# Kernel tuning notes

Hardware: AMD Instinct MI355X
Metric: run time of the kernel (lower is better)

Reference implementation:

```python
import jax, jax.numpy as jnp
import numpy as np

BLOCK_SIZE = 64


def setup_inputs() -> dict:
    key = jax.random.key(0)
    kq, kk, kv, km = jax.random.split(key, 4)
    H, N, D = 16, 8192, 64
    nb = N // BLOCK_SIZE
    return {
        "q": jax.random.normal(kq, (H, N, D), dtype=jnp.float32),
        "k": jax.random.normal(kk, (H, N, D), dtype=jnp.float32),
        "v": jax.random.normal(kv, (H, N, D), dtype=jnp.float32),
        "block_mask": jax.random.randint(km, (nb, nb), 0, 2, dtype=jnp.int32),
    }


def reference(q, k, v, block_mask):
    """Block-sparse flash attention with online softmax.

    q, k, v: [H, N, D]; block_mask: [N//B, N//B] (1 = valid, 0 = masked).
    Scans over key blocks, processing all query rows at once; masked blocks
    contribute exactly zero (exp(-inf) = 0), matching the original's skip.
    """
    H, N, D = q.shape
    B = BLOCK_SIZE
    nb = N // B
    scale = D ** -0.5

    kb = k.reshape(H, nb, B, D).transpose(1, 0, 2, 3)  # [nb, H, B, D]
    vb = v.reshape(H, nb, B, D).transpose(1, 0, 2, 3)  # [nb, H, B, D]
    mask_cols = block_mask.T  # [nb_key, nb_query]: row j = validity of key block j per query block

    m0 = jnp.full((H, N, 1), -jnp.inf, dtype=q.dtype)
    l0 = jnp.zeros((H, N, 1), dtype=q.dtype)
    o0 = jnp.zeros((H, N, D), dtype=q.dtype)

    def step(carry, xs):
        m, l, o = carry
        k_j, v_j, mcol = xs  # k_j/v_j: [H, B, D]; mcol: [nb] over query blocks
        logits = jnp.einsum('hnd,hbd->hnb', q, k_j) * scale  # [H, N, B]
        valid = (jnp.repeat(mcol, B) > 0)[None, :, None]      # [1, N, 1]
        logits = jnp.where(valid, logits, -jnp.inf)
        m_new = jnp.maximum(m, logits.max(-1, keepdims=True))
        # guard: if everything so far is masked, m_new = -inf; use 0 to keep exps finite (=0)
        m_safe = jnp.where(jnp.isneginf(m_new), jnp.zeros_like(m_new), m_new)
        a_old = jnp.exp(m - m_safe)       # rescale of previous accumulators
        p = jnp.exp(logits - m_safe)      # masked entries -> 0
        l = a_old * l + p.sum(-1, keepdims=True)
        o = a_old * o + jnp.einsum('hnb,hbd->hnd', p, v_j)
        return (m_new, l, o), None

    (m, l, o), _ = jax.lax.scan(step, (m0, l0, o0), (kb, vb, mask_cols))
    return o / l
```

## Files before the change

### kernel.cpp

```cpp
#include <hip/hip_runtime.h>
#include <hip/hip_bf16.h>

#define Hh 16
#define Nn 8192
#define Dd 64
#define NB 128

typedef float  f32x4   __attribute__((ext_vector_type(4)));
typedef float  f32x16  __attribute__((ext_vector_type(16)));
typedef float  float4_ __attribute__((ext_vector_type(4)));
typedef short  bf16x8  __attribute__((ext_vector_type(8)));
typedef unsigned short ushort8  __attribute__((ext_vector_type(8)));
typedef unsigned short ushort4_ __attribute__((ext_vector_type(4)));

typedef const __attribute__((address_space(1))) unsigned int gu32;
typedef __attribute__((address_space(3))) unsigned int lu32;

#define QSCALE 0.1803368801111244f

__device__ __forceinline__ unsigned short f2bf(float f) {
    union { float f; unsigned u; } x; x.f = f;
    unsigned r = x.u + 0x7fffu + ((x.u >> 16) & 1u);
    return (unsigned short)(r >> 16);
}

__device__ __forceinline__ unsigned packbf2(float lo, float hi) {
    __hip_bfloat162 h2 = __float22bfloat162_rn(make_float2(lo, hi));
    unsigned u; __builtin_memcpy(&u, &h2, 4);
    return u;
}

__global__ void cvt_k(const float* __restrict__ k, unsigned short* __restrict__ ko) {
    int i = blockIdx.x * 256 + threadIdx.x;
    float4_ b = ((const float4_*)k)[i];
    ushort4_ ob;
#pragma unroll
    for (int j = 0; j < 4; ++j) ob[j] = f2bf(b[j]);
    ((ushort4_*)ko)[i] = ob;
}

__global__ void cvt_vt(const float* __restrict__ v, unsigned short* __restrict__ vt) {
    int jb = blockIdx.x, h = blockIdx.y, t = threadIdx.x;
    __shared__ float T[64][65];
    const float4_* src = (const float4_*)(v + ((long)h * Nn + jb * 64) * Dd);
#pragma unroll
    for (int it = 0; it < 4; ++it) {
        int r = (t >> 4) + it * 16;
        int c0 = (t & 15) * 4;
        float4_ x = src[r * 16 + (t & 15)];
#pragma unroll
        for (int i2 = 0; i2 < 4; ++i2) T[c0 + i2][r] = x[i2];
    }
    __syncthreads();
    int d = t >> 2, seg = (t & 3) * 16;
    ushort8 o0, o1;
#pragma unroll
    for (int i2 = 0; i2 < 8; ++i2) o0[i2] = f2bf(T[d][seg + i2]);
#pragma unroll
    for (int i2 = 0; i2 < 8; ++i2) o1[i2] = f2bf(T[d][seg + 8 + i2]);
    unsigned short* dst = vt + (((size_t)h * NB + jb) * Dd + d) * 64 + seg;
    *(ushort8*)dst = o0;
    *(ushort8*)(dst + 8) = o1;
}

__global__ __launch_bounds__(256, 2) void attn32(
        const unsigned short* __restrict__ k16,
        const unsigned short* __restrict__ vt16,
        const float* __restrict__ qf,
        const int* __restrict__ mask,
        float* __restrict__ out) {
    int bid = blockIdx.x;
    int h = (bid & 7) | ((bid >> 9) << 3);
    int qb2 = (bid >> 3) & 63;
    int tid = threadIdx.x;
    int wid = tid >> 6, l = tid & 63;
    int q5 = l & 31, hi = l >> 5;
    int pair = wid >> 1;
    int kvrole = wid & 1;

    __shared__ unsigned short Kl[2][2][4096];
    __shared__ unsigned short Vl[2][2][4096];

    const int* mrowA = mask + (qb2 * 2) * NB;
    const int* mrowB = mask + (qb2 * 2 + 1) * NB;
    unsigned long long a_lo = __ballot(mrowA[l] != 0);
    unsigned long long a_hi = __ballot(mrowA[64 + l] != 0);
    unsigned long long c_lo = __ballot(mrowB[l] != 0);
    unsigned long long c_hi = __ballot(mrowB[64 + l] != 0);
    int cntA = __popcll(a_lo) + __popcll(a_hi);
    int cntB = __popcll(c_lo) + __popcll(c_hi);
    int maxcnt = cntA > cntB ? cntA : cntB;

    if (maxcnt == 0) {
        float4_ z = {0.f, 0.f, 0.f, 0.f};
        float4_* ob = (float4_*)(out + ((size_t)h * Nn + qb2 * 128) * Dd);
        for (int x = tid; x < 128 * 64 / 4; x += 256) ob[x] = z;
        return;
    }

    int cnt_own = pair ? cntB : cntA;
    unsigned long long r0 = pair ? c_lo : a_lo;
    unsigned long long r1 = pair ? c_hi : a_hi;

    size_t qrow = (size_t)h * Nn + qb2 * 128 + pair * 64 + kvrole * 32 + q5;
    bf16x8 qfrag[4];
#pragma unroll
    for (int ds_ = 0; ds_ < 4; ++ds_) {
        const float4_* qs = (const float4_*)(qf + qrow * Dd + ds_ * 16 + hi * 8);
        float4_ x = qs[0], y = qs[1];
        union { unsigned u[4]; bf16x8 v; } u;
        u.u[0] = packbf2(x[0] * QSCALE, x[1] * QSCALE);
        u.u[1] = packbf2(x[2] * QSCALE, x[3] * QSCALE);
        u.u[2] = packbf2(y[0] * QSCALE, y[1] * QSCALE);
        u.u[3] = packbf2(y[2] * QSCALE, y[3] * QSCALE);
        qfrag[ds_] = u.v;
    }

    union { unsigned short s[8]; bf16x8 v; } ones;
#pragma unroll
    for (int i2 = 0; i2 < 8; ++i2) ones.s[i2] = 0x3F80;

    const unsigned short* sp[8];
#pragma unroll
    for (int f = 0; f < 8; ++f) {
        if (kvrole == 0)
            sp[f] = k16 + (size_t)h * (Nn * Dd)
                  + (size_t)(q5 + 32 * (f >> 2)) * Dd + (f & 3) * 16 + hi * 8;
        else
            sp[f] = vt16 + (size_t)h * (Nn * Dd)
                  + (size_t)(q5 + 32 * (f >> 2)) * 64 + (f & 3) * 16 + hi * 8;
    }
    const int jmul = 64 * Dd;

    auto next_j = [&]() {
        int jj;
        if (r0)      { jj = __ffsll(r0) - 1; r0 &= r0 - 1; }
        else if (r1) { jj = 63 + __ffsll(r1); r1 &= r1 - 1; }
        else         { jj = 0; }
        return jj;
    };

    auto issue = [&](int nbuf, int jj) {
        unsigned short* lb = (kvrole == 0) ? &Kl[pair][nbuf][0] : &Vl[pair][nbuf][0];
#pragma unroll
        for (int f = 0; f < 8; ++f) {
            const unsigned short* g = sp[f] + (size_t)jj * jmul;
            __builtin_amdgcn_global_load_lds((gu32*)g, (lu32*)(lb + f * 512), 16, 0, 0);
        }
    };

    issue(0, next_j());

    f32x16 o0 = {}, o1 = {}, ls = {};

    for (int i = 0; i < maxcnt; ++i) {
        int buf = i & 1;
        __syncthreads();
        if (i + 1 < maxcnt) issue(buf ^ 1, next_j());

        unsigned msk = (i < cnt_own) ? 0xFFFFFFFFu : 0u;

        const char* kb = (const char*)&Kl[pair][buf][0] + l * 16;
        const char* vb = (const char*)&Vl[pair][buf][0] + l * 16;

        f32x16 s0 = {}, s1 = {};
#pragma unroll
        for (int ds_ = 0; ds_ < 4; ++ds_) {
            bf16x8 kf0 = *(const bf16x8*)(kb + ds_ * 1024);
            s0 = __builtin_amdgcn_mfma_f32_32x32x16_bf16(kf0, qfrag[ds_], s0, 0, 0, 0);
        }
#pragma unroll
        for (int ds_ = 0; ds_ < 4; ++ds_) {
            bf16x8 kf1 = *(const bf16x8*)(kb + 4096 + ds_ * 1024);
            s1 = __builtin_amdgcn_mfma_f32_32x32x16_bf16(kf1, qfrag[ds_], s1, 0, 0, 0);
        }

#pragma unroll
        for (int e = 0; e < 16; ++e) s0[e] = __builtin_amdgcn_exp2f(s0[e]);
#pragma unroll
        for (int e = 0; e < 16; ++e) s1[e] = __builtin_amdgcn_exp2f(s1[e]);

        unsigned w0[8], w1[8];
#pragma unroll
        for (int jj = 0; jj < 8; ++jj) {
            w0[jj] = packbf2(s0[2 * jj], s0[2 * jj + 1]) & msk;
            w1[jj] = packbf2(s1[2 * jj], s1[2 * jj + 1]) & msk;
        }
        auto swap32 = [&](unsigned& a, unsigned& b) {
            unsigned send = hi ? a : b;
            unsigned recv = (unsigned)__shfl_xor((int)send, 32);
            a = hi ? recv : a;
            b = hi ? b : recv;
        };
        swap32(w0[0], w0[2]); swap32(w0[1], w0[3]);
        swap32(w0[4], w0[6]); swap32(w0[5], w0[7]);
        swap32(w1[0], w1[2]); swap32(w1[1], w1[3]);
        swap32(w1[4], w1[6]); swap32(w1[5], w1[7]);

        union U { unsigned u[4]; bf16x8 v; };
        U pbs[4];
        pbs[0].u[0] = w0[0]; pbs[0].u[1] = w0[1]; pbs[0].u[2] = w0[2]; pbs[0].u[3] = w0[3];
        pbs[1].u[0] = w0[4]; pbs[1].u[1] = w0[5]; pbs[1].u[2] = w0[6]; pbs[1].u[3] = w0[7];
        pbs[2].u[0] = w1[0]; pbs[2].u[1] = w1[1]; pbs[2].u[2] = w1[2]; pbs[2].u[3] = w1[3];
        pbs[3].u[0] = w1[4]; pbs[3].u[1] = w1[5]; pbs[3].u[2] = w1[6]; pbs[3].u[3] = w1[7];

#pragma unroll
        for (int c = 0; c < 4; ++c) {
            bf16x8 vf0 = *(const bf16x8*)(vb + c * 1024);
            o0 = __builtin_amdgcn_mfma_f32_32x32x16_bf16(vf0, pbs[c].v, o0, 0, 0, 0);
        }
#pragma unroll
        for (int c = 0; c < 4; ++c) {
            bf16x8 vf1 = *(const bf16x8*)(vb + 4096 + c * 1024);
            o1 = __builtin_amdgcn_mfma_f32_32x32x16_bf16(vf1, pbs[c].v, o1, 0, 0, 0);
        }
#pragma unroll
        for (int c = 0; c < 4; ++c)
            ls = __builtin_amdgcn_mfma_f32_32x32x16_bf16(ones.v, pbs[c].v, ls, 0, 0, 0);
    }

    float inv = cnt_own ? (1.0f / ls[0]) : 0.f;
    float* obase = out + qrow * Dd;
#pragma unroll
    for (int s4 = 0; s4 < 4; ++s4) {
        float4_ t0, t1;
#pragma unroll
        for (int e = 0; e < 4; ++e) { t0[e] = o0[4 * s4 + e] * inv; t1[e] = o1[4 * s4 + e] * inv; }
        *(float4_*)(obase + 8 * s4 + 4 * hi)      = t0;
        *(float4_*)(obase + 32 + 8 * s4 + 4 * hi) = t1;
    }
}

__global__ void attn_main(const float* __restrict__ qf, const float* __restrict__ kf,
                          const float* __restrict__ vf, const int* __restrict__ mask,
                          float* __restrict__ out) {
    int id = blockIdx.x;
    int h = id & 15, qb = id >> 4;
    int tid = threadIdx.x;
    int lane = tid & 63, wid = tid >> 6;
    int l15 = lane & 15, l4 = lane >> 4;

    __shared__ unsigned short Kl[2][64 * 64];
    __shared__ unsigned short Vl[2][64 * 64];
    __shared__ unsigned short Pl[4][16 * 64];

    const int* mrow = mask + qb * NB;
    unsigned long long b0 = __ballot(mrow[lane] != 0);
    unsigned long long b1 = __ballot(mrow[64 + lane] != 0);
    int count = __popcll(b0) + __popcll(b1);

    float* op = out + ((long)h * Nn + qb * 64 + wid * 16) * Dd;

    if (count == 0) {
#pragma unroll
        for (int r = 0; r < 4; ++r)
#pragma unroll
            for (int dn = 0; dn < 4; ++dn)
                op[(l4 * 4 + r) * Dd + dn * 16 + l15] = 0.f;
        return;
    }

    long qrow = (long)h * Nn + qb * 64 + wid * 16 + l15;
    bf16x8 qfrag[2];
#pragma unroll
    for (int dc = 0; dc < 2; ++dc) {
        const float4_* qs = (const float4_*)qf + qrow * 16 + dc * 8 + l4 * 2;
        float4_ x = qs[0], y = qs[1];
        union { unsigned short s[8]; bf16x8 v; } u;
#pragma unroll
        for (int i2 = 0; i2 < 4; ++i2) {
            u.s[i2] = f2bf(x[i2] * 0.125f);
            u.s[4 + i2] = f2bf(y[i2] * 0.125f);
        }
        qfrag[dc] = u.v;
    }

    int sgq = tid & 7;
    int srow = tid >> 3;
    float4_ kf4[2][2]; float4_ vf4[4];
    int vk = tid & 63, vd0 = (tid >> 6) * 16;

    auto load_kv = [&](int j) {
        const float4_* ks = (const float4_*)kf + ((long)h * Nn + j * 64) * 16;
#pragma unroll
        for (int it = 0; it < 2; ++it) {
            kf4[it][0] = ks[(srow + it * 32) * 16 + sgq * 2];
            kf4[it][1] = ks[(srow + it * 32) * 16 + sgq * 2 + 1];
        }
        const float4_* vs = (const float4_*)vf + ((long)h * Nn + j * 64) * 16;
#pragma unroll
        for (int c = 0; c < 4; ++c) vf4[c] = vs[vk * 16 + (vd0 >> 2) + c];
    };

    auto write_kv = [&](int buf) {
#pragma unroll
        for (int it = 0; it < 2; ++it) {
            int r = srow + it * 32;
            union { unsigned short s[8]; ushort8 v; } u;
#pragma unroll
            for (int i2 = 0; i2 < 4; ++i2) {
                u.s[i2] = f2bf(kf4[it][0][i2]);
                u.s[4 + i2] = f2bf(kf4[it][1][i2]);
            }
            *(ushort8*)((char*)&Kl[buf][0] + r * 128 + (((sgq ^ r) & 7) << 4)) = u.v;
        }
#pragma unroll
        for (int i2 = 0; i2 < 16; ++i2) {
            int d = vd0 + i2;
            *((unsigned short*)((char*)&Vl[buf][0] + d * 128 +
                ((((vk >> 3) ^ d) & 7) << 4) + ((vk & 7) << 1))) = f2bf(vf4[i2 >> 2][i2 & 3]);
        }
    };

    f32x4 o_acc[4] = {};
    float m_r[4], l_r[4];
#pragma unroll
    for (int r = 0; r < 4; ++r) { m_r[r] = -INFINITY; l_r[r] = 0.f; }

    unsigned long long r0 = b0, r1 = b1;
    auto next_j = [&]() {
        int jj;
        if (r0) { jj = __ffsll(r0) - 1; r0 &= r0 - 1; }
        else    { jj = 63 + __ffsll(r1); r1 &= r1 - 1; }
        return jj;
    };

    load_kv(next_j());

    for (int i = 0; i < count; ++i) {
        int buf = i & 1;
        write_kv(buf);
        __syncthreads();
        if (i + 1 < count) load_kv(next_j());

        f32x4 s[4] = {};
#pragma unroll
        for (int dc = 0; dc < 2; ++dc) {
#pragma unroll
            for (int kn = 0; kn < 4; ++kn) {
                int krow = kn * 16 + l15;
                bf16x8 kfr = *(const bf16x8*)((const char*)&Kl[buf][0] +
                               krow * 128 + ((((l4 + dc * 4) ^ krow) & 7) << 4));
                s[kn] = __builtin_amdgcn_mfma_f32_16x16x32_bf16(qfrag[dc], kfr, s[kn], 0, 0, 0);
            }
        }

#pragma unroll
        for (int r = 0; r < 4; ++r) {
            float mx = fmaxf(fmaxf(s[0][r], s[1][r]), fmaxf(s[2][r], s[3][r]));
#pragma unroll
            for (int off = 1; off < 16; off <<= 1) mx = fmaxf(mx, __shfl_xor(mx, off));
            float mn = fmaxf(m_r[r], mx);
            float a = __expf(m_r[r] - mn);
            m_r[r] = mn;
            float psum = 0.f;
#pragma unroll
            for (int kn = 0; kn < 4; ++kn) { float p = __expf(s[kn][r] - mn); s[kn][r] = p; psum += p; }
#pragma unroll
            for (int off = 1; off < 16; off <<= 1) psum += __shfl_xor(psum, off);
            l_r[r] = l_r[r] * a + psum;
            o_acc[0][r] *= a; o_acc[1][r] *= a; o_acc[2][r] *= a; o_acc[3][r] *= a;
        }

#pragma unroll
        for (int kn = 0; kn < 4; ++kn) {
#pragma unroll
            for (int r = 0; r < 4; ++r) {
                int prow = l4 * 4 + r;
                int pc = kn * 16 + l15;
                *((unsigned short*)((char*)&Pl[wid][0] + prow * 128 +
                    ((((pc >> 3) ^ prow) & 7) << 4) + ((pc & 7) << 1))) = f2bf(s[kn][r]);
            }
        }

        bf16x8 pa[2];
#pragma unroll
        for (int kc = 0; kc < 2; ++kc)
            pa[kc] = *(const bf16x8*)((const char*)&Pl[wid][0] +
                      l15 * 128 + ((((l4 + kc * 4) ^ l15) & 7) << 4));
#pragma unroll
        for (int dn = 0; dn < 4; ++dn) {
            int vrow = dn * 16 + l15;
#pragma unroll
            for (int kc = 0; kc < 2; ++kc) {
                bf16x8 vbf = *(const bf16x8*)((const char*)&Vl[buf][0] +
                             vrow * 128 + ((((l4 + kc * 4) ^ vrow) & 7) << 4));
                o_acc[dn] = __builtin_amdgcn_mfma_f32_16x16x32_bf16(pa[kc], vbf, o_acc[dn], 0, 0, 0);
            }
        }
    }

#pragma unroll
    for (int r = 0; r < 4; ++r) {
        float inv = 1.0f / l_r[r];
#pragma unroll
        for (int dn = 0; dn < 4; ++dn)
            op[(l4 * 4 + r) * Dd + dn * 16 + l15] = o_acc[dn][r] * inv;
    }
}

extern "C" void kernel_launch(void* const* d_in, const int* in_sizes, int n_in,
                              void* d_out, int out_size, void* d_ws, size_t ws_size,
                              hipStream_t stream) {
    const float* q = (const float*)d_in[0];
    const float* k = (const float*)d_in[1];
    const float* v = (const float*)d_in[2];
    const int* mask = (const int*)d_in[3];
    float* out = (float*)d_out;

    size_t elems = (size_t)Hh * Nn * Dd;
    size_t need = 2 * elems * sizeof(unsigned short);
    if (ws_size >= need) {
        unsigned short* k16 = (unsigned short*)d_ws;
        unsigned short* vt16 = k16 + elems;
        cvt_k<<<dim3((unsigned)(elems / 1024)), 256, 0, stream>>>(k, k16);
        cvt_vt<<<dim3(NB, Hh), 256, 0, stream>>>(v, vt16);
        attn32<<<dim3(Hh * NB / 2), 256, 0, stream>>>(k16, vt16, q, mask, out);
    } else {
        attn_main<<<dim3(Hh * NB), 256, 0, stream>>>(q, k, v, mask, out);
    }
}
```

Before: 288.9 us.

## Split attention blocks to one query block per workgroup, drop LDS double buffering

Each 128-thread workgroup now handles a single 64-row query block instead of two paired blocks in a 256-thread workgroup. This removes the padding work that occurs when two query blocks have different mask counts. The K/V tiles now use a single LDS buffer, with the next load issued after compute and a second barrier. That gives up the overlap between the next tile's load and the current MFMA work in exchange for less LDS, smaller workgroups and more of them resident.

```diff
diff --git a/kernel.cpp b/kernel.cpp
--- a/kernel.cpp
+++ b/kernel.cpp
@@ -63,46 +63,36 @@
     *(ushort8*)(dst + 8) = o1;
 }
 
-__global__ __launch_bounds__(256, 2) void attn32(
+__global__ __launch_bounds__(128, 4) void attn32(
         const unsigned short* __restrict__ k16,
         const unsigned short* __restrict__ vt16,
         const float* __restrict__ qf,
         const int* __restrict__ mask,
         float* __restrict__ out) {
     int bid = blockIdx.x;
-    int h = (bid & 7) | ((bid >> 9) << 3);
-    int qb2 = (bid >> 3) & 63;
+    int h = (bid & 7) | ((bid >> 10) << 3);
+    int qb = (bid >> 3) & 127;
     int tid = threadIdx.x;
     int wid = tid >> 6, l = tid & 63;
     int q5 = l & 31, hi = l >> 5;
-    int pair = wid >> 1;
-    int kvrole = wid & 1;
-
-    __shared__ unsigned short Kl[2][2][4096];
-    __shared__ unsigned short Vl[2][2][4096];
-
-    const int* mrowA = mask + (qb2 * 2) * NB;
-    const int* mrowB = mask + (qb2 * 2 + 1) * NB;
-    unsigned long long a_lo = __ballot(mrowA[l] != 0);
-    unsigned long long a_hi = __ballot(mrowA[64 + l] != 0);
-    unsigned long long c_lo = __ballot(mrowB[l] != 0);
-    unsigned long long c_hi = __ballot(mrowB[64 + l] != 0);
-    int cntA = __popcll(a_lo) + __popcll(a_hi);
-    int cntB = __popcll(c_lo) + __popcll(c_hi);
-    int maxcnt = cntA > cntB ? cntA : cntB;
-
-    if (maxcnt == 0) {
+
+    __shared__ unsigned short Kl[4096];
+    __shared__ unsigned short Vl[4096];
+
+    const int* mrow = mask + qb * NB;
+    unsigned long long b0 = __ballot(mrow[l] != 0);
+    unsigned long long b1 = __ballot(mrow[64 + l] != 0);
+    int count = __popcll(b0) + __popcll(b1);
+
+    size_t qrow = (size_t)h * Nn + qb * 64 + wid * 32 + q5;
+
+    if (count == 0) {
         float4_ z = {0.f, 0.f, 0.f, 0.f};
-        float4_* ob = (float4_*)(out + ((size_t)h * Nn + qb2 * 128) * Dd);
-        for (int x = tid; x < 128 * 64 / 4; x += 256) ob[x] = z;
+        float4_* ob = (float4_*)(out + ((size_t)h * Nn + qb * 64) * Dd);
+        for (int x = tid; x < 64 * 64 / 4; x += 128) ob[x] = z;
         return;
     }
 
-    int cnt_own = pair ? cntB : cntA;
-    unsigned long long r0 = pair ? c_lo : a_lo;
-    unsigned long long r1 = pair ? c_hi : a_hi;
-
-    size_t qrow = (size_t)h * Nn + qb2 * 128 + pair * 64 + kvrole * 32 + q5;
     bf16x8 qfrag[4];
 #pragma unroll
     for (int ds_ = 0; ds_ < 4; ++ds_) {
@@ -123,7 +113,7 @@
     const unsigned short* sp[8];
 #pragma unroll
     for (int f = 0; f < 8; ++f) {
-        if (kvrole == 0)
+        if (wid == 0)
             sp[f] = k16 + (size_t)h * (Nn * Dd)
                   + (size_t)(q5 + 32 * (f >> 2)) * Dd + (f & 3) * 16 + hi * 8;
         else
@@ -132,16 +122,16 @@
     }
     const int jmul = 64 * Dd;
 
+    unsigned long long r0 = b0, r1 = b1;
     auto next_j = [&]() {
         int jj;
-        if (r0)      { jj = __ffsll(r0) - 1; r0 &= r0 - 1; }
-        else if (r1) { jj = 63 + __ffsll(r1); r1 &= r1 - 1; }
-        else         { jj = 0; }
+        if (r0) { jj = __ffsll(r0) - 1; r0 &= r0 - 1; }
+        else    { jj = 63 + __ffsll(r1); r1 &= r1 - 1; }
         return jj;
     };
 
-    auto issue = [&](int nbuf, int jj) {
-        unsigned short* lb = (kvrole == 0) ? &Kl[pair][nbuf][0] : &Vl[pair][nbuf][0];
+    auto issue = [&](int jj) {
+        unsigned short* lb = (wid == 0) ? &Kl[0] : &Vl[0];
 #pragma unroll
         for (int f = 0; f < 8; ++f) {
             const unsigned short* g = sp[f] + (size_t)jj * jmul;
@@ -149,19 +139,15 @@
         }
     };
 
-    issue(0, next_j());
+    issue(next_j());
 
     f32x16 o0 = {}, o1 = {}, ls = {};
 
-    for (int i = 0; i < maxcnt; ++i) {
-        int buf = i & 1;
+    for (int i = 0; i < count; ++i) {
         __syncthreads();
-        if (i + 1 < maxcnt) issue(buf ^ 1, next_j());
-
-        unsigned msk = (i < cnt_own) ? 0xFFFFFFFFu : 0u;
-
-        const char* kb = (const char*)&Kl[pair][buf][0] + l * 16;
-        const char* vb = (const char*)&Vl[pair][buf][0] + l * 16;
+
+        const char* kb = (const char*)&Kl[0] + l * 16;
+        const char* vb = (const char*)&Vl[0] + l * 16;
 
         f32x16 s0 = {}, s1 = {};
 #pragma unroll
@@ -183,8 +169,8 @@
         unsigned w0[8], w1[8];
 #pragma unroll
         for (int jj = 0; jj < 8; ++jj) {
-            w0[jj] = packbf2(s0[2 * jj], s0[2 * jj + 1]) & msk;
-            w1[jj] = packbf2(s1[2 * jj], s1[2 * jj + 1]) & msk;
+            w0[jj] = packbf2(s0[2 * jj], s0[2 * jj + 1]);
+            w1[jj] = packbf2(s1[2 * jj], s1[2 * jj + 1]);
         }
         auto swap32 = [&](unsigned& a, unsigned& b) {
             unsigned send = hi ? a : b;
@@ -217,9 +203,12 @@
 #pragma unroll
         for (int c = 0; c < 4; ++c)
             ls = __builtin_amdgcn_mfma_f32_32x32x16_bf16(ones.v, pbs[c].v, ls, 0, 0, 0);
-    }
-
-    float inv = cnt_own ? (1.0f / ls[0]) : 0.f;
+
+        __syncthreads();
+        if (i + 1 < count) issue(next_j());
+    }
+
+    float inv = 1.0f / ls[0];
     float* obase = out + qrow * Dd;
 #pragma unroll
     for (int s4 = 0; s4 < 4; ++s4) {
@@ -415,7 +404,7 @@
         unsigned short* vt16 = k16 + elems;
         cvt_k<<<dim3((unsigned)(elems / 1024)), 256, 0, stream>>>(k, k16);
         cvt_vt<<<dim3(NB, Hh), 256, 0, stream>>>(v, vt16);
-        attn32<<<dim3(Hh * NB / 2), 256, 0, stream>>>(k16, vt16, q, mask, out);
+        attn32<<<dim3(Hh * NB), 128, 0, stream>>>(k16, vt16, q, mask, out);
     } else {
         attn_main<<<dim3(Hh * NB), 256, 0, stream>>>(q, k, v, mask, out);
     }
```

New measurement: 319.4 us. +10.6%, slower.

## Split key blocks into 32-key halves to halve LDS and raise occupancy

Applied to the files above, without the earlier changes.

The attn32 kernel now processes each 64-key block as two 32-key sub-steps. This halves the K/V shared-memory buffers, live score registers and P fragments, and launch bounds rise from 2 to 4 blocks per CU. The aim is more concurrent waves to hide memory and MFMA latency. The cost is twice as many loop iterations, so twice as many __syncthreads barriers and async issue points per key block, with smaller loads per step.

```diff
diff --git a/kernel.cpp b/kernel.cpp
--- a/kernel.cpp
+++ b/kernel.cpp
@@ -63,7 +63,7 @@
     *(ushort8*)(dst + 8) = o1;
 }
 
-__global__ __launch_bounds__(256, 2) void attn32(
+__global__ __launch_bounds__(256, 4) void attn32(
         const unsigned short* __restrict__ k16,
         const unsigned short* __restrict__ vt16,
         const float* __restrict__ qf,
@@ -78,8 +78,8 @@
     int pair = wid >> 1;
     int kvrole = wid & 1;
 
-    __shared__ unsigned short Kl[2][2][4096];
-    __shared__ unsigned short Vl[2][2][4096];
+    __shared__ unsigned short Kl[2][2][2048];
+    __shared__ unsigned short Vl[2][2][2048];
 
     const int* mrowA = mask + (qb2 * 2) * NB;
     const int* mrowB = mask + (qb2 * 2 + 1) * NB;
@@ -98,7 +98,8 @@
         return;
     }
 
-    int cnt_own = pair ? cntB : cntA;
+    int cnt_own2 = 2 * (pair ? cntB : cntA);
+    int maxcnt2 = 2 * maxcnt;
     unsigned long long r0 = pair ? c_lo : a_lo;
     unsigned long long r1 = pair ? c_hi : a_hi;
 
@@ -120,72 +121,68 @@
 #pragma unroll
     for (int i2 = 0; i2 < 8; ++i2) ones.s[i2] = 0x3F80;
 
-    const unsigned short* sp[8];
-#pragma unroll
-    for (int f = 0; f < 8; ++f) {
+    const unsigned short* sp[4];
+#pragma unroll
+    for (int f = 0; f < 4; ++f) {
         if (kvrole == 0)
             sp[f] = k16 + (size_t)h * (Nn * Dd)
-                  + (size_t)(q5 + 32 * (f >> 2)) * Dd + (f & 3) * 16 + hi * 8;
+                  + (size_t)q5 * Dd + f * 16 + hi * 8;
         else
             sp[f] = vt16 + (size_t)h * (Nn * Dd)
-                  + (size_t)(q5 + 32 * (f >> 2)) * 64 + (f & 3) * 16 + hi * 8;
-    }
-    const int jmul = 64 * Dd;
-
-    auto next_j = [&]() {
-        int jj;
-        if (r0)      { jj = __ffsll(r0) - 1; r0 &= r0 - 1; }
-        else if (r1) { jj = 63 + __ffsll(r1); r1 &= r1 - 1; }
-        else         { jj = 0; }
-        return jj;
+                  + (size_t)(q5 + 32 * (f >> 1)) * 64 + (f & 1) * 16 + hi * 8;
+    }
+
+    int hold_j = 0, sub = 0;
+    auto next_off = [&]() -> size_t {
+        if (sub == 0) {
+            if (r0)      { hold_j = __ffsll(r0) - 1; r0 &= r0 - 1; }
+            else if (r1) { hold_j = 63 + __ffsll(r1); r1 &= r1 - 1; }
+            else         { hold_j = 0; }
+            sub = 1;
+            return (size_t)hold_j * 4096;
+        } else {
+            sub = 0;
+            return (size_t)hold_j * 4096 + (kvrole == 0 ? 2048u : 32u);
+        }
     };
 
-    auto issue = [&](int nbuf, int jj) {
+    auto issue = [&](int nbuf, size_t off) {
         unsigned short* lb = (kvrole == 0) ? &Kl[pair][nbuf][0] : &Vl[pair][nbuf][0];
 #pragma unroll
-        for (int f = 0; f < 8; ++f) {
-            const unsigned short* g = sp[f] + (size_t)jj * jmul;
+        for (int f = 0; f < 4; ++f) {
+            const unsigned short* g = sp[f] + off;
             __builtin_amdgcn_global_load_lds((gu32*)g, (lu32*)(lb + f * 512), 16, 0, 0);
         }
     };
 
-    issue(0, next_j());
+    issue(0, next_off());
 
     f32x16 o0 = {}, o1 = {}, ls = {};
 
-    for (int i = 0; i < maxcnt; ++i) {
+    for (int i = 0; i < maxcnt2; ++i) {
         int buf = i & 1;
         __syncthreads();
-        if (i + 1 < maxcnt) issue(buf ^ 1, next_j());
-
-        unsigned msk = (i < cnt_own) ? 0xFFFFFFFFu : 0u;
+        if (i + 1 < maxcnt2) issue(buf ^ 1, next_off());
+
+        unsigned msk = (i < cnt_own2) ? 0xFFFFFFFFu : 0u;
 
         const char* kb = (const char*)&Kl[pair][buf][0] + l * 16;
         const char* vb = (const char*)&Vl[pair][buf][0] + l * 16;
 
-        f32x16 s0 = {}, s1 = {};
+        f32x16 s0 = {};
 #pragma unroll
         for (int ds_ = 0; ds_ < 4; ++ds_) {
             bf16x8 kf0 = *(const bf16x8*)(kb + ds_ * 1024);
             s0 = __builtin_amdgcn_mfma_f32_32x32x16_bf16(kf0, qfrag[ds_], s0, 0, 0, 0);
         }
-#pragma unroll
-        for (int ds_ = 0; ds_ < 4; ++ds_) {
-            bf16x8 kf1 = *(const bf16x8*)(kb + 4096 + ds_ * 1024);
-            s1 = __builtin_amdgcn_mfma_f32_32x32x16_bf16(kf1, qfrag[ds_], s1, 0, 0, 0);
-        }
 
 #pragma unroll
         for (int e = 0; e < 16; ++e) s0[e] = __builtin_amdgcn_exp2f(s0[e]);
-#pragma unroll
-        for (int e = 0; e < 16; ++e) s1[e] = __builtin_amdgcn_exp2f(s1[e]);
-
-        unsigned w0[8], w1[8];
-#pragma unroll
-        for (int jj = 0; jj < 8; ++jj) {
+
+        unsigned w0[8];
+#pragma unroll
+        for (int jj = 0; jj < 8; ++jj)
             w0[jj] = packbf2(s0[2 * jj], s0[2 * jj + 1]) & msk;
-            w1[jj] = packbf2(s1[2 * jj], s1[2 * jj + 1]) & msk;
-        }
         auto swap32 = [&](unsigned& a, unsigned& b) {
             unsigned send = hi ? a : b;
             unsigned recv = (unsigned)__shfl_xor((int)send, 32);
@@ -194,32 +191,27 @@
         };
         swap32(w0[0], w0[2]); swap32(w0[1], w0[3]);
         swap32(w0[4], w0[6]); swap32(w0[5], w0[7]);
-        swap32(w1[0], w1[2]); swap32(w1[1], w1[3]);
-        swap32(w1[4], w1[6]); swap32(w1[5], w1[7]);
 
         union U { unsigned u[4]; bf16x8 v; };
-        U pbs[4];
+        U pbs[2];
         pbs[0].u[0] = w0[0]; pbs[0].u[1] = w0[1]; pbs[0].u[2] = w0[2]; pbs[0].u[3] = w0[3];
         pbs[1].u[0] = w0[4]; pbs[1].u[1] = w0[5]; pbs[1].u[2] = w0[6]; pbs[1].u[3] = w0[7];
-        pbs[2].u[0] = w1[0]; pbs[2].u[1] = w1[1]; pbs[2].u[2] = w1[2]; pbs[2].u[3] = w1[3];
-        pbs[3].u[0] = w1[4]; pbs[3].u[1] = w1[5]; pbs[3].u[2] = w1[6]; pbs[3].u[3] = w1[7];
-
-#pragma unroll
-        for (int c = 0; c < 4; ++c) {
+
+#pragma unroll
+        for (int c = 0; c < 2; ++c) {
             bf16x8 vf0 = *(const bf16x8*)(vb + c * 1024);
             o0 = __builtin_amdgcn_mfma_f32_32x32x16_bf16(vf0, pbs[c].v, o0, 0, 0, 0);
         }
 #pragma unroll
-        for (int c = 0; c < 4; ++c) {
-            bf16x8 vf1 = *(const bf16x8*)(vb + 4096 + c * 1024);
+        for (int c = 0; c < 2; ++c) {
+            bf16x8 vf1 = *(const bf16x8*)(vb + 2048 + c * 1024);
             o1 = __builtin_amdgcn_mfma_f32_32x32x16_bf16(vf1, pbs[c].v, o1, 0, 0, 0);
         }
-#pragma unroll
-        for (int c = 0; c < 4; ++c)
-            ls = __builtin_amdgcn_mfma_f32_32x32x16_bf16(ones.v, pbs[c].v, ls, 0, 0, 0);
-    }
-
-    float inv = cnt_own ? (1.0f / ls[0]) : 0.f;
+        ls = __builtin_amdgcn_mfma_f32_32x32x16_bf16(ones.v, pbs[0].v, ls, 0, 0, 0);
+        ls = __builtin_amdgcn_mfma_f32_32x32x16_bf16(ones.v, pbs[1].v, ls, 0, 0, 0);
+    }
+
+    float inv = cnt_own2 ? (1.0f / ls[0]) : 0.f;
     float* obase = out + qrow * Dd;
 #pragma unroll
     for (int s4 = 0; s4 < 4; ++s4) {
```

Result: slower. 300.0 us (+3.9%).

## Load V fragments directly from global into registers, halve LDS and raise occupancy

Applied to the files above, without the earlier changes.

V tiles are no longer staged through LDS. Each wave reads its V fragments straight from global memory into registers every iteration, and the K staging work is split across both waves of a pair. This halves shared memory use, so launch bounds go from 2 to 4 blocks per CU to raise occupancy. The cost is that the direct V loads are not prefetched and sit on the critical path just before the PV MFMAs, with each wave loading the full V tile redundantly.

```diff
diff --git a/kernel.cpp b/kernel.cpp
--- a/kernel.cpp
+++ b/kernel.cpp
@@ -63,7 +63,7 @@
     *(ushort8*)(dst + 8) = o1;
 }
 
-__global__ __launch_bounds__(256, 2) void attn32(
+__global__ __launch_bounds__(256, 4) void attn32(
         const unsigned short* __restrict__ k16,
         const unsigned short* __restrict__ vt16,
         const float* __restrict__ qf,
@@ -79,7 +79,6 @@
     int kvrole = wid & 1;
 
     __shared__ unsigned short Kl[2][2][4096];
-    __shared__ unsigned short Vl[2][2][4096];
 
     const int* mrowA = mask + (qb2 * 2) * NB;
     const int* mrowB = mask + (qb2 * 2 + 1) * NB;
@@ -120,16 +119,19 @@
 #pragma unroll
     for (int i2 = 0; i2 < 8; ++i2) ones.s[i2] = 0x3F80;
 
-    const unsigned short* sp[8];
-#pragma unroll
-    for (int f = 0; f < 8; ++f) {
-        if (kvrole == 0)
-            sp[f] = k16 + (size_t)h * (Nn * Dd)
-                  + (size_t)(q5 + 32 * (f >> 2)) * Dd + (f & 3) * 16 + hi * 8;
-        else
-            sp[f] = vt16 + (size_t)h * (Nn * Dd)
-                  + (size_t)(q5 + 32 * (f >> 2)) * 64 + (f & 3) * 16 + hi * 8;
-    }
+    const unsigned short* sp[4];
+#pragma unroll
+    for (int ff = 0; ff < 4; ++ff) {
+        int f = kvrole * 4 + ff;
+        sp[ff] = k16 + (size_t)h * (Nn * Dd)
+               + (size_t)(q5 + 32 * (f >> 2)) * Dd + (f & 3) * 16 + hi * 8;
+    }
+    const unsigned short* vbase = vt16 + (size_t)h * (Nn * Dd);
+    int voff[8];
+#pragma unroll
+    for (int f = 0; f < 8; ++f)
+        voff[f] = (q5 + 32 * (f >> 2)) * 64 + (f & 3) * 16 + hi * 8;
+
     const int jmul = 64 * Dd;
 
     auto next_j = [&]() {
@@ -141,27 +143,38 @@
     };
 
     auto issue = [&](int nbuf, int jj) {
-        unsigned short* lb = (kvrole == 0) ? &Kl[pair][nbuf][0] : &Vl[pair][nbuf][0];
-#pragma unroll
-        for (int f = 0; f < 8; ++f) {
-            const unsigned short* g = sp[f] + (size_t)jj * jmul;
-            __builtin_amdgcn_global_load_lds((gu32*)g, (lu32*)(lb + f * 512), 16, 0, 0);
+        unsigned short* lb = &Kl[pair][nbuf][0];
+#pragma unroll
+        for (int ff = 0; ff < 4; ++ff) {
+            const unsigned short* g = sp[ff] + (size_t)jj * jmul;
+            __builtin_amdgcn_global_load_lds((gu32*)g,
+                (lu32*)(lb + (kvrole * 4 + ff) * 512), 16, 0, 0);
         }
     };
 
-    issue(0, next_j());
+    int jcur = next_j();
+    issue(0, jcur);
 
     f32x16 o0 = {}, o1 = {}, ls = {};
 
     for (int i = 0; i < maxcnt; ++i) {
         int buf = i & 1;
         __syncthreads();
-        if (i + 1 < maxcnt) issue(buf ^ 1, next_j());
+        int jnext = 0;
+        if (i + 1 < maxcnt) { jnext = next_j(); issue(buf ^ 1, jnext); }
+
+        bf16x8 vreg[8];
+        {
+            const unsigned short* vj = vbase + (size_t)jcur * jmul;
+#pragma unroll
+            for (int f = 0; f < 8; ++f)
+                vreg[f] = *(const bf16x8*)(vj + voff[f]);
+        }
+        jcur = jnext;
 
         unsigned msk = (i < cnt_own) ? 0xFFFFFFFFu : 0u;
 
         const char* kb = (const char*)&Kl[pair][buf][0] + l * 16;
-        const char* vb = (const char*)&Vl[pair][buf][0] + l * 16;
 
         f32x16 s0 = {}, s1 = {};
 #pragma unroll
@@ -205,15 +218,11 @@
         pbs[3].u[0] = w1[4]; pbs[3].u[1] = w1[5]; pbs[3].u[2] = w1[6]; pbs[3].u[3] = w1[7];
 
 #pragma unroll
-        for (int c = 0; c < 4; ++c) {
-            bf16x8 vf0 = *(const bf16x8*)(vb + c * 1024);
-            o0 = __builtin_amdgcn_mfma_f32_32x32x16_bf16(vf0, pbs[c].v, o0, 0, 0, 0);
-        }
-#pragma unroll
-        for (int c = 0; c < 4; ++c) {
-            bf16x8 vf1 = *(const bf16x8*)(vb + 4096 + c * 1024);
-            o1 = __builtin_amdgcn_mfma_f32_32x32x16_bf16(vf1, pbs[c].v, o1, 0, 0, 0);
-        }
+        for (int c = 0; c < 4; ++c)
+            o0 = __builtin_amdgcn_mfma_f32_32x32x16_bf16(vreg[c], pbs[c].v, o0, 0, 0, 0);
+#pragma unroll
+        for (int c = 0; c < 4; ++c)
+            o1 = __builtin_amdgcn_mfma_f32_32x32x16_bf16(vreg[4 + c], pbs[c].v, o1, 0, 0, 0);
 #pragma unroll
         for (int c = 0; c < 4; ++c)
             ls = __builtin_amdgcn_mfma_f32_32x32x16_bf16(ones.v, pbs[c].v, ls, 0, 0, 0);
```

After: 422.8 us. 1.46x slower.
